# Optimization experiments

Measured on AMD Instinct MI355X. Metric: run time of the kernel, lower is better.

## Reference

```python
import jax, jax.numpy as jnp
import numpy as np


def setup_inputs() -> dict:
    key = jax.random.key(0)
    k1, k2, k3, k4 = jax.random.split(key, 4)
    B, C, H, Wd = 32, 512, 32, 32
    sparse_dim, dict_size, feature_dim = 1024, 1024, 512
    x = jax.random.normal(k1, (B, C, H, Wd), dtype=jnp.float32)
    dictionary = jax.random.normal(k2, (dict_size, feature_dim), dtype=jnp.float32)
    # scale W, S like the LISTA init (|| . || ~ O(1)) so iterates stay bounded
    W = jax.random.normal(k3, (sparse_dim, feature_dim), dtype=jnp.float32) * 0.02
    S = jax.random.normal(k4, (sparse_dim, sparse_dim), dtype=jnp.float32) * 0.02
    thresh = jnp.float32(0.1)
    return {"x": x, "dictionary": dictionary, "W": W, "S": S, "thresh": thresh, "num_steps": 5}


def _soft_threshold(z, thresh):
    return jnp.sign(z) * jnp.maximum(jnp.abs(z) - thresh, 0.0)


def reference(x, dictionary, W, S, thresh, num_steps):
    B, C, H, Wd = x.shape
    sparse_dim = S.shape[0]
    # [B,C,H,W] -> [B*H*W, C]
    x_flat = jnp.transpose(x, (0, 2, 3, 1)).reshape(-1, C)
    dict_norm = dictionary / jnp.linalg.norm(dictionary, axis=1, keepdims=True)
    # W @ x^T is loop-invariant; compute once. [K, N]
    Wx = W @ x_flat.T
    z = jnp.zeros((sparse_dim, x_flat.shape[0]), dtype=x.dtype)
    for _ in range(num_steps):
        z = z + Wx
        z = z - S @ z
        z = _soft_threshold(z, thresh)
    # [K,N] -> [B,K,H,W]
    z = jnp.transpose(z.T.reshape(B, H, Wd, sparse_dim), (0, 3, 1, 2))
    return (z, dict_norm)
```

## Files before the change

### kernel.cpp

```cpp
#include <hip/hip_runtime.h>
#include <hip/hip_bf16.h>

typedef __bf16 bf16_t;
typedef __bf16 bf16x4 __attribute__((ext_vector_type(4)));
typedef __bf16 bf16x8 __attribute__((ext_vector_type(8)));
typedef float f32x4 __attribute__((ext_vector_type(4)));

#define GLOAD_LDS16(g, l)                                                      \
  __builtin_amdgcn_global_load_lds(                                            \
      (const __attribute__((address_space(1))) void*)(g),                      \
      (__attribute__((address_space(3))) void*)(l), 16, 0, 0)

#define MFMA(a, b, c) __builtin_amdgcn_mfma_f32_16x16x32_bf16((a), (b), (c), 0, 0, 0)

__global__ __launch_bounds__(256, 2) void gemm_kernel(
    const bf16_t* __restrict__ A, const bf16_t* __restrict__ Bt,
    int Kd, int mode,
    const bf16_t* __restrict__ WxIn, bf16_t* __restrict__ UnextOrWx,
    float* __restrict__ Out, const float* __restrict__ thresh_p)
{
  __shared__ __align__(16) char smem[73728];
  bf16_t* lds = (bf16_t*)smem;

  const int tid = threadIdx.x;
  const int wid = tid >> 6, lane = tid & 63;
  const int wr = wid >> 1, wc = wid & 1;
  const int lr = lane & 15, kg = lane >> 4;

  const int per = gridDim.x >> 3;
  const int logical = (blockIdx.x & 7) * per + (blockIdx.x >> 3);
  const int tileN = (logical & 7) << 7;
  const int tileM = (logical >> 3) << 8;
  const int NT = Kd >> 5;

  size_t offA[4]; int dstA[4];
  #pragma unroll
  for (int j = 0; j < 4; ++j) {
    const int f = j * 256 + tid;
    const int row = f >> 2, u = f & 3;
    const int ug = u ^ ((row >> 1) & 3);
    offA[j] = (size_t)(tileM + row) * Kd + ug * 8;
    dstA[j] = f * 8;
  }
  size_t offB[2]; int dstB[2];
  #pragma unroll
  for (int j = 0; j < 2; ++j) {
    const int f = j * 256 + tid;
    const int col = f >> 2, u = f & 3;
    const int ug = u ^ ((col >> 1) & 3);
    offB[j] = (size_t)(tileN + col) * Kd + ug * 8;
    dstB[j] = 8192 + f * 8;
  }

  auto readA = [&](int mi, int bs) -> bf16x8 {
    const int R = wr * 128 + mi * 16 + lr;
    return *(const bf16x8*)(lds + bs + R * 32 + ((kg ^ ((R >> 1) & 3)) << 3));
  };
  auto readB = [&](int ni, int bs) -> bf16x8 {
    const int C = wc * 64 + ni * 16 + lr;
    return *(const bf16x8*)(lds + bs + 8192 + C * 32 + ((kg ^ ((C >> 1) & 3)) << 3));
  };

  f32x4 acc[8][4] = {};
  bf16x8 af[4], bfr[4];

  #pragma unroll
  for (int j = 0; j < 4; ++j) GLOAD_LDS16(A + offA[j], lds + dstA[j]);
  #pragma unroll
  for (int j = 0; j < 2; ++j) GLOAD_LDS16(Bt + offB[j], lds + dstB[j]);
  #pragma unroll
  for (int j = 0; j < 4; ++j) GLOAD_LDS16(A + offA[j] + 32, lds + 12288 + dstA[j]);
  #pragma unroll
  for (int j = 0; j < 2; ++j) GLOAD_LDS16(Bt + offB[j] + 32, lds + 12288 + dstB[j]);
  asm volatile("s_waitcnt vmcnt(6)" ::: "memory");
  __builtin_amdgcn_s_barrier();

  int buf = 0, sb3 = 2;
  for (int t = 0; t < NT; ++t) {
    const int bs = buf * 12288;
    const int sbs = sb3 * 12288;
    const int ts = (t + 2 < NT) ? t + 2 : t + 2 - NT;
    const size_t ko = (size_t)ts << 5;

    #pragma unroll
    for (int mi = 0; mi < 4; ++mi) af[mi] = readA(mi, bs);
    #pragma unroll
    for (int ni = 0; ni < 4; ++ni) bfr[ni] = readB(ni, bs);
    GLOAD_LDS16(A + offA[0] + ko, lds + sbs + dstA[0]);
    GLOAD_LDS16(A + offA[1] + ko, lds + sbs + dstA[1]);
    GLOAD_LDS16(A + offA[2] + ko, lds + sbs + dstA[2]);
    __builtin_amdgcn_s_barrier();
    asm volatile("s_waitcnt lgkmcnt(0)" ::: "memory");
    __builtin_amdgcn_sched_barrier(0);
    __builtin_amdgcn_s_setprio(1);
    #pragma unroll
    for (int mi = 0; mi < 4; ++mi)
      #pragma unroll
      for (int ni = 0; ni < 4; ++ni)
        acc[mi][ni] = MFMA(af[mi], bfr[ni], acc[mi][ni]);
    __builtin_amdgcn_s_setprio(0);

    #pragma unroll
    for (int mi = 0; mi < 4; ++mi) af[mi] = readA(mi + 4, bs);
    GLOAD_LDS16(A + offA[3] + ko, lds + sbs + dstA[3]);
    GLOAD_LDS16(Bt + offB[0] + ko, lds + sbs + dstB[0]);
    GLOAD_LDS16(Bt + offB[1] + ko, lds + sbs + dstB[1]);
    __builtin_amdgcn_s_barrier();
    asm volatile("s_waitcnt lgkmcnt(0)" ::: "memory");
    __builtin_amdgcn_sched_barrier(0);
    __builtin_amdgcn_s_setprio(1);
    #pragma unroll
    for (int mi = 0; mi < 4; ++mi)
      #pragma unroll
      for (int ni = 0; ni < 4; ++ni)
        acc[mi + 4][ni] = MFMA(af[mi], bfr[ni], acc[mi + 4][ni]);
    __builtin_amdgcn_s_setprio(0);
    asm volatile("s_waitcnt vmcnt(6)" ::: "memory");
    __builtin_amdgcn_s_barrier();

    buf = (buf == 2) ? 0 : buf + 1;
    sb3 = (sb3 == 2) ? 0 : sb3 + 1;
  }

  const float th = *thresh_p;

  if (mode <= 1) {
    asm volatile("s_waitcnt vmcnt(0)" ::: "memory");
    __syncthreads();
    float* Tl = (float*)smem;
    #pragma unroll
    for (int c = 0; c < 8; ++c) {
      if (c) __syncthreads();
      if (wr == (c >> 2)) {
        #pragma unroll
        for (int mj = 0; mj < 2; ++mj) {
          const int mi = (c & 3) * 2 + mj;
          const int rl = mj * 16 + kg * 4;
          #pragma unroll
          for (int ni = 0; ni < 4; ++ni) {
            const int cl = wc * 64 + ni * 16 + lr;
            #pragma unroll
            for (int r = 0; r < 4; ++r)
              Tl[(rl + r) * 132 + cl] = acc[mi][ni][r];
          }
        }
      }
      __syncthreads();
      #pragma unroll
      for (int j = 0; j < 4; ++j) {
        const int f  = j * 256 + tid;
        const int rl = f >> 5;
        const int c4 = (f & 31) * 4;
        const f32x4 v = *(const f32x4*)&Tl[rl * 132 + c4];
        const int grow = tileM + c * 32 + rl;
        const size_t gidx = (size_t)grow * 1024 + tileN + c4;
        bf16x4 ov;
        if (mode == 1) {
          const bf16x4 wx = *(const bf16x4*)&WxIn[gidx];
          #pragma unroll
          for (int e = 0; e < 4; ++e) {
            const float a  = fabsf(v[e]) - th;
            const float zn = (a > 0.f) ? copysignf(a, v[e]) : 0.f;
            ov[e] = (bf16_t)(zn + (float)wx[e]);
          }
        } else {
          #pragma unroll
          for (int e = 0; e < 4; ++e) ov[e] = (bf16_t)v[e];
        }
        *(bf16x4*)&UnextOrWx[gidx] = ov;
      }
    }
  } else {
    #pragma unroll
    for (int mi = 0; mi < 8; ++mi)
      #pragma unroll
      for (int ni = 0; ni < 4; ++ni)
        #pragma unroll
        for (int r = 0; r < 4; ++r) {
          const float v = acc[mi][ni][r];
          const float a = fabsf(v) - th;
          acc[mi][ni][r] = (a > 0.f) ? copysignf(a, v) : 0.f;
        }
    asm volatile("s_waitcnt vmcnt(0)" ::: "memory");
    __syncthreads();
    float* T = (float*)smem;
    const int    bb    = tileM >> 10;
    const size_t obase = (size_t)bb * 1048576 + (size_t)(tileM & 1023);
    #pragma unroll
    for (int ch = 0; ch < 4; ++ch) {
      if (ch) __syncthreads();
      if (wc == (ch >> 1)) {
        #pragma unroll
        for (int nj = 0; nj < 2; ++nj) {
          const int ni = (ch & 1) * 2 + nj;
          const int cp = nj * 16 + lr;
          #pragma unroll
          for (int mi = 0; mi < 8; ++mi)
            #pragma unroll
            for (int r = 0; r < 4; ++r)
              T[cp * 260 + wr * 128 + mi * 16 + kg * 4 + r] = acc[mi][ni][r];
        }
      }
      __syncthreads();
      #pragma unroll
      for (int j = 0; j < 8; ++j) {
        const int f  = j * 256 + tid;
        const int cp = f >> 6;
        const int p4 = (f & 63) * 4;
        const f32x4 v = *(const f32x4*)&T[cp * 260 + p4];
        *(f32x4*)&Out[obase + (size_t)(tileN + ch * 32 + cp) * 1024 + p4] = v;
      }
    }
  }
}

__global__ void cast_f32_bf16_kernel(const float* __restrict__ src,
                                     bf16_t* __restrict__ dst, int n) {
  int i = blockIdx.x * blockDim.x + threadIdx.x;
  if (i < n) dst[i] = (bf16_t)src[i];
}

__global__ void make_T_kernel(const float* __restrict__ S,
                              bf16_t* __restrict__ T) {
  const int idx = blockIdx.x * blockDim.x + threadIdx.x;
  const int i = idx >> 10, j = idx & 1023;
  T[idx] = (bf16_t)(((i == j) ? 1.0f : 0.0f) - S[idx]);
}

__global__ void transpose_cast_x_kernel(const float* __restrict__ x,
                                        bf16_t* __restrict__ xt) {
  __shared__ float t[32][33];
  const int b  = blockIdx.z;
  const int p0 = blockIdx.x * 32;
  const int c0 = blockIdx.y * 32;
  const int tx = threadIdx.x, ty = threadIdx.y;
  #pragma unroll
  for (int i = 0; i < 32; i += 8)
    t[ty + i][tx] = x[((size_t)b * 512 + c0 + ty + i) * 1024 + p0 + tx];
  __syncthreads();
  #pragma unroll
  for (int i = 0; i < 32; i += 8)
    xt[((size_t)b * 1024 + p0 + ty + i) * 512 + c0 + tx] = (bf16_t)t[tx][ty + i];
}

__global__ void dict_norm_kernel(const float* __restrict__ dict,
                                 float* __restrict__ out) {
  const int row = blockIdx.x;
  const int tid = threadIdx.x;
  const float* r = dict + (size_t)row * 512;
  float s = 0.f;
  for (int i = tid; i < 512; i += 256) { float v = r[i]; s += v * v; }
  #pragma unroll
  for (int off = 32; off > 0; off >>= 1) s += __shfl_down(s, off);
  __shared__ float ps[4];
  if ((tid & 63) == 0) ps[tid >> 6] = s;
  __syncthreads();
  const float inv = 1.0f / sqrtf(ps[0] + ps[1] + ps[2] + ps[3]);
  for (int i = tid; i < 512; i += 256) out[(size_t)row * 512 + i] = r[i] * inv;
}

extern "C" void kernel_launch(void* const* d_in, const int* in_sizes, int n_in,
                              void* d_out, int out_size, void* d_ws, size_t ws_size,
                              hipStream_t stream) {
  const float* x      = (const float*)d_in[0];
  const float* dict   = (const float*)d_in[1];
  const float* W      = (const float*)d_in[2];
  const float* S      = (const float*)d_in[3];
  const float* thresh = (const float*)d_in[4];

  float* out = (float*)d_out;

  char* ws = (char*)d_ws;
  bf16_t* uA   = (bf16_t*)ws;
  bf16_t* uB   = (bf16_t*)(ws + 67108864);
  bf16_t* WxBf = (bf16_t*)(ws + 134217728);
  bf16_t* xt   = (bf16_t*)(ws + 201326592);
  bf16_t* Wbf  = (bf16_t*)(ws + 234881024);
  bf16_t* Tbf  = (bf16_t*)(ws + 235929600);

  float* dnorm = out + 33554432;

  cast_f32_bf16_kernel<<<dim3(2048), dim3(256), 0, stream>>>(W, Wbf, 524288);
  make_T_kernel<<<dim3(2048), dim3(512), 0, stream>>>(S, Tbf);
  transpose_cast_x_kernel<<<dim3(32, 16, 32), dim3(32, 8), 0, stream>>>(x, xt);
  dict_norm_kernel<<<dim3(1024), dim3(256), 0, stream>>>(dict, dnorm);

  gemm_kernel<<<dim3(1024), dim3(256), 0, stream>>>(
      xt, Wbf, 512, 0, nullptr, WxBf, nullptr, thresh);

  bf16_t* uc = WxBf; bf16_t* un = uA;
  for (int s = 0; s < 4; ++s) {
    gemm_kernel<<<dim3(1024), dim3(256), 0, stream>>>(
        uc, Tbf, 1024, 1, WxBf, un, nullptr, thresh);
    uc = un;
    un = (uc == uA) ? uB : uA;
  }
  gemm_kernel<<<dim3(1024), dim3(256), 0, stream>>>(
      uc, Tbf, 1024, 2, nullptr, nullptr, out, thresh);
}
```

Before: 595.2 us.

## Use 512-thread blocks with eight waves each computing a 64x64 sub-tile

Each 256x128 GEMM block tile is now split across eight waves instead of four, so every wave holds a 64x64 accumulator instead of 128x64. Loads per thread drop to three per K-step, and the main loop becomes one phase: issue prefetch, read fragments, run 16 MFMAs, one barrier. This removes the two-phase interleave and the s_setprio hints. The epilogues are remapped to the new wave layout. The aim is to cut register pressure and raise waves per CU to hide memory latency better, at the cost of losing the hand-tuned MFMA/load interleave. The 72KB of LDS per block may also cap resident blocks below the new launch bound.

```diff
diff --git a/kernel.cpp b/kernel.cpp
--- a/kernel.cpp
+++ b/kernel.cpp
@@ -13,7 +13,7 @@
 
 #define MFMA(a, b, c) __builtin_amdgcn_mfma_f32_16x16x32_bf16((a), (b), (c), 0, 0, 0)
 
-__global__ __launch_bounds__(256, 2) void gemm_kernel(
+__global__ __launch_bounds__(512, 4) void gemm_kernel(
     const bf16_t* __restrict__ A, const bf16_t* __restrict__ Bt,
     int Kd, int mode,
     const bf16_t* __restrict__ WxIn, bf16_t* __restrict__ UnextOrWx,
@@ -33,27 +33,25 @@
   const int tileM = (logical >> 3) << 8;
   const int NT = Kd >> 5;
 
-  size_t offA[4]; int dstA[4];
-  #pragma unroll
-  for (int j = 0; j < 4; ++j) {
-    const int f = j * 256 + tid;
+  size_t offA[2]; int dstA[2];
+  #pragma unroll
+  for (int j = 0; j < 2; ++j) {
+    const int f = j * 512 + tid;
     const int row = f >> 2, u = f & 3;
     const int ug = u ^ ((row >> 1) & 3);
     offA[j] = (size_t)(tileM + row) * Kd + ug * 8;
     dstA[j] = f * 8;
   }
-  size_t offB[2]; int dstB[2];
-  #pragma unroll
-  for (int j = 0; j < 2; ++j) {
-    const int f = j * 256 + tid;
-    const int col = f >> 2, u = f & 3;
+  size_t offB; int dstB;
+  {
+    const int col = tid >> 2, u = tid & 3;
     const int ug = u ^ ((col >> 1) & 3);
-    offB[j] = (size_t)(tileN + col) * Kd + ug * 8;
-    dstB[j] = 8192 + f * 8;
+    offB = (size_t)(tileN + col) * Kd + ug * 8;
+    dstB = 8192 + tid * 8;
   }
 
   auto readA = [&](int mi, int bs) -> bf16x8 {
-    const int R = wr * 128 + mi * 16 + lr;
+    const int R = wr * 64 + mi * 16 + lr;
     return *(const bf16x8*)(lds + bs + R * 32 + ((kg ^ ((R >> 1) & 3)) << 3));
   };
   auto readB = [&](int ni, int bs) -> bf16x8 {
@@ -61,18 +59,16 @@
     return *(const bf16x8*)(lds + bs + 8192 + C * 32 + ((kg ^ ((C >> 1) & 3)) << 3));
   };
 
-  f32x4 acc[8][4] = {};
+  f32x4 acc[4][4] = {};
   bf16x8 af[4], bfr[4];
 
-  #pragma unroll
-  for (int j = 0; j < 4; ++j) GLOAD_LDS16(A + offA[j], lds + dstA[j]);
-  #pragma unroll
-  for (int j = 0; j < 2; ++j) GLOAD_LDS16(Bt + offB[j], lds + dstB[j]);
-  #pragma unroll
-  for (int j = 0; j < 4; ++j) GLOAD_LDS16(A + offA[j] + 32, lds + 12288 + dstA[j]);
-  #pragma unroll
-  for (int j = 0; j < 2; ++j) GLOAD_LDS16(Bt + offB[j] + 32, lds + 12288 + dstB[j]);
-  asm volatile("s_waitcnt vmcnt(6)" ::: "memory");
+  GLOAD_LDS16(A + offA[0], lds + dstA[0]);
+  GLOAD_LDS16(A + offA[1], lds + dstA[1]);
+  GLOAD_LDS16(Bt + offB, lds + dstB);
+  GLOAD_LDS16(A + offA[0] + 32, lds + 12288 + dstA[0]);
+  GLOAD_LDS16(A + offA[1] + 32, lds + 12288 + dstA[1]);
+  GLOAD_LDS16(Bt + offB + 32, lds + 12288 + dstB);
+  asm volatile("s_waitcnt vmcnt(3)" ::: "memory");
   __builtin_amdgcn_s_barrier();
 
   int buf = 0, sb3 = 2;
@@ -82,40 +78,22 @@
     const int ts = (t + 2 < NT) ? t + 2 : t + 2 - NT;
     const size_t ko = (size_t)ts << 5;
 
-    #pragma unroll
-    for (int mi = 0; mi < 4; ++mi) af[mi] = readA(mi, bs);
-    #pragma unroll
-    for (int ni = 0; ni < 4; ++ni) bfr[ni] = readB(ni, bs);
     GLOAD_LDS16(A + offA[0] + ko, lds + sbs + dstA[0]);
     GLOAD_LDS16(A + offA[1] + ko, lds + sbs + dstA[1]);
-    GLOAD_LDS16(A + offA[2] + ko, lds + sbs + dstA[2]);
-    __builtin_amdgcn_s_barrier();
-    asm volatile("s_waitcnt lgkmcnt(0)" ::: "memory");
-    __builtin_amdgcn_sched_barrier(0);
-    __builtin_amdgcn_s_setprio(1);
+    GLOAD_LDS16(Bt + offB + ko, lds + sbs + dstB);
+
+    #pragma unroll
+    for (int mi = 0; mi < 4; ++mi) af[mi] = readA(mi, bs);
+    #pragma unroll
+    for (int ni = 0; ni < 4; ++ni) bfr[ni] = readB(ni, bs);
+
     #pragma unroll
     for (int mi = 0; mi < 4; ++mi)
       #pragma unroll
       for (int ni = 0; ni < 4; ++ni)
         acc[mi][ni] = MFMA(af[mi], bfr[ni], acc[mi][ni]);
-    __builtin_amdgcn_s_setprio(0);
-
-    #pragma unroll
-    for (int mi = 0; mi < 4; ++mi) af[mi] = readA(mi + 4, bs);
-    GLOAD_LDS16(A + offA[3] + ko, lds + sbs + dstA[3]);
-    GLOAD_LDS16(Bt + offB[0] + ko, lds + sbs + dstB[0]);
-    GLOAD_LDS16(Bt + offB[1] + ko, lds + sbs + dstB[1]);
-    __builtin_amdgcn_s_barrier();
-    asm volatile("s_waitcnt lgkmcnt(0)" ::: "memory");
-    __builtin_amdgcn_sched_barrier(0);
-    __builtin_amdgcn_s_setprio(1);
-    #pragma unroll
-    for (int mi = 0; mi < 4; ++mi)
-      #pragma unroll
-      for (int ni = 0; ni < 4; ++ni)
-        acc[mi + 4][ni] = MFMA(af[mi], bfr[ni], acc[mi + 4][ni]);
-    __builtin_amdgcn_s_setprio(0);
-    asm volatile("s_waitcnt vmcnt(6)" ::: "memory");
+
+    asm volatile("s_waitcnt vmcnt(3)" ::: "memory");
     __builtin_amdgcn_s_barrier();
 
     buf = (buf == 2) ? 0 : buf + 1;
@@ -131,10 +109,10 @@
     #pragma unroll
     for (int c = 0; c < 8; ++c) {
       if (c) __syncthreads();
-      if (wr == (c >> 2)) {
+      if (wr == (c >> 1)) {
         #pragma unroll
         for (int mj = 0; mj < 2; ++mj) {
-          const int mi = (c & 3) * 2 + mj;
+          const int mi = (c & 1) * 2 + mj;
           const int rl = mj * 16 + kg * 4;
           #pragma unroll
           for (int ni = 0; ni < 4; ++ni) {
@@ -147,8 +125,8 @@
       }
       __syncthreads();
       #pragma unroll
-      for (int j = 0; j < 4; ++j) {
-        const int f  = j * 256 + tid;
+      for (int j = 0; j < 2; ++j) {
+        const int f  = j * 512 + tid;
         const int rl = f >> 5;
         const int c4 = (f & 31) * 4;
         const f32x4 v = *(const f32x4*)&Tl[rl * 132 + c4];
@@ -172,7 +150,7 @@
     }
   } else {
     #pragma unroll
-    for (int mi = 0; mi < 8; ++mi)
+    for (int mi = 0; mi < 4; ++mi)
       #pragma unroll
       for (int ni = 0; ni < 4; ++ni)
         #pragma unroll
@@ -195,16 +173,16 @@
           const int ni = (ch & 1) * 2 + nj;
           const int cp = nj * 16 + lr;
           #pragma unroll
-          for (int mi = 0; mi < 8; ++mi)
+          for (int mi = 0; mi < 4; ++mi)
             #pragma unroll
             for (int r = 0; r < 4; ++r)
-              T[cp * 260 + wr * 128 + mi * 16 + kg * 4 + r] = acc[mi][ni][r];
+              T[cp * 260 + wr * 64 + mi * 16 + kg * 4 + r] = acc[mi][ni][r];
         }
       }
       __syncthreads();
       #pragma unroll
-      for (int j = 0; j < 8; ++j) {
-        const int f  = j * 256 + tid;
+      for (int j = 0; j < 4; ++j) {
+        const int f  = j * 512 + tid;
         const int cp = f >> 6;
         const int p4 = (f & 63) * 4;
         const f32x4 v = *(const f32x4*)&T[cp * 260 + p4];
@@ -285,16 +263,16 @@
   transpose_cast_x_kernel<<<dim3(32, 16, 32), dim3(32, 8), 0, stream>>>(x, xt);
   dict_norm_kernel<<<dim3(1024), dim3(256), 0, stream>>>(dict, dnorm);
 
-  gemm_kernel<<<dim3(1024), dim3(256), 0, stream>>>(
+  gemm_kernel<<<dim3(1024), dim3(512), 0, stream>>>(
       xt, Wbf, 512, 0, nullptr, WxBf, nullptr, thresh);
 
   bf16_t* uc = WxBf; bf16_t* un = uA;
   for (int s = 0; s < 4; ++s) {
-    gemm_kernel<<<dim3(1024), dim3(256), 0, stream>>>(
+    gemm_kernel<<<dim3(1024), dim3(512), 0, stream>>>(
         uc, Tbf, 1024, 1, WxBf, un, nullptr, thresh);
     uc = un;
     un = (uc == uA) ? uB : uA;
   }
-  gemm_kernel<<<dim3(1024), dim3(256), 0, stream>>>(
+  gemm_kernel<<<dim3(1024), dim3(512), 0, stream>>>(
       uc, Tbf, 1024, 2, nullptr, nullptr, out, thresh);
 }
```

New measurement: 551.0 us. 1.08x faster.
